# Optimization experiments

Hardware: AMD Instinct MI355X
Metric: run time of the kernel (lower is better)

## Reference

```python
import jax, jax.numpy as jnp
import numpy as np

LAYER_NUMS = 3


def setup_inputs() -> dict:
    key = jax.random.key(0)
    k1, k2 = jax.random.split(key)
    B, D = 8192, 1024
    x = jax.random.normal(k1, (B, D), dtype=jnp.float32)
    W = jax.random.normal(k2, (LAYER_NUMS, D), dtype=jnp.float32)
    b = jnp.zeros((LAYER_NUMS, D), dtype=jnp.float32)
    return {"x": x, "W": W, "b": b}


def reference(x, W, b):
    # DCN cross layer: x_{l+1} = x_0 * (x_l . w_l) + b_l + x_l
    # The torch code materializes the [B,d,d] outer product x_0 x_l^T then
    # contracts with w; algebraically identical to scaling x_0 by the
    # scalar dot product (x_l . w), which we compute directly.
    x0 = x
    x_l = x
    for i in range(LAYER_NUMS):
        scale = jnp.einsum('bd,d->b', x_l, W[i])       # [B]
        x_l = x0 * scale[:, None] + b[i][None, :] + x_l  # [B, d]
    return x_l
```

## Files before the change

### kernel.cpp

```cpp
#include <hip/hip_runtime.h>


#define DDIM 1024
#define LAYERS 3

__global__ __launch_bounds__(256) void CrossLayer_kernel(
    const float* __restrict__ x,
    const float* __restrict__ W,
    const float* __restrict__ bias,
    float* __restrict__ out,
    int B)
{
    const int wave = threadIdx.x >> 6;
    const int lane = threadIdx.x & 63;
    const int row  = blockIdx.x * 4 + wave;
    if (row >= B) return;

    const float4* xrow = reinterpret_cast<const float4*>(x + (size_t)row * DDIM);

    float4 x0[4], xl[4];
#pragma unroll
    for (int c = 0; c < 4; ++c) {
        x0[c] = xrow[c * 64 + lane];
        xl[c] = x0[c];
    }

#pragma unroll
    for (int l = 0; l < LAYERS; ++l) {
        const float4* wrow = reinterpret_cast<const float4*>(W    + l * DDIM);
        const float4* brow = reinterpret_cast<const float4*>(bias + l * DDIM);

        float partial = 0.f;
#pragma unroll
        for (int c = 0; c < 4; ++c) {
            float4 w = wrow[c * 64 + lane];
            partial += xl[c].x * w.x + xl[c].y * w.y
                     + xl[c].z * w.z + xl[c].w * w.w;
        }
#pragma unroll
        for (int off = 32; off > 0; off >>= 1)
            partial += __shfl_xor(partial, off, 64);
        const float scale = partial;

#pragma unroll
        for (int c = 0; c < 4; ++c) {
            float4 bv = brow[c * 64 + lane];
            xl[c].x = fmaf(x0[c].x, scale, bv.x + xl[c].x);
            xl[c].y = fmaf(x0[c].y, scale, bv.y + xl[c].y);
            xl[c].z = fmaf(x0[c].z, scale, bv.z + xl[c].z);
            xl[c].w = fmaf(x0[c].w, scale, bv.w + xl[c].w);
        }
    }

    float4* orow = reinterpret_cast<float4*>(out + (size_t)row * DDIM);
#pragma unroll
    for (int c = 0; c < 4; ++c)
        orow[c * 64 + lane] = xl[c];
}

extern "C" void kernel_launch(void* const* d_in, const int* in_sizes, int n_in,
                              void* d_out, int out_size, void* d_ws, size_t ws_size,
                              hipStream_t stream) {
    const float* x  = (const float*)d_in[0];
    const float* W  = (const float*)d_in[1];
    const float* b  = (const float*)d_in[2];
    float* out      = (float*)d_out;

    const int B = in_sizes[0] / DDIM;
    dim3 grid((B + 3) / 4), block(256);
    hipLaunchKernelGGL(CrossLayer_kernel, grid, block, 0, stream,
                       x, W, b, out, B);
}
```

Before: 17.53 us.

## Collapse three cross layers into one fused reduction and closed-form scale

Rewrites the layer recurrence algebraically: x_l stays of the form alpha*x0 + partial bias sums, so all three dot products (x0·w_i and the bias·w terms) are computed in one pass and reduced together. The three serialized wave reductions become one interleaved set of shuffles, and the final output is a single FMA with a summed bias. Output stores are marked nontemporal. Floating-point rounding changes slightly from the reordered arithmetic, and the bias vectors are now loaded twice.

```diff
diff --git a/kernel.cpp b/kernel.cpp
--- a/kernel.cpp
+++ b/kernel.cpp
@@ -3,6 +3,8 @@
 
 #define DDIM 1024
 #define LAYERS 3
+
+typedef float f32x4 __attribute__((ext_vector_type(4)));
 
 __global__ __launch_bounds__(256) void CrossLayer_kernel(
     const float* __restrict__ x,
@@ -16,46 +18,64 @@
     const int row  = blockIdx.x * 4 + wave;
     if (row >= B) return;
 
-    const float4* xrow = reinterpret_cast<const float4*>(x + (size_t)row * DDIM);
+    const f32x4* xrow = reinterpret_cast<const f32x4*>(x + (size_t)row * DDIM);
+    const f32x4* w0   = reinterpret_cast<const f32x4*>(W);
+    const f32x4* w1   = reinterpret_cast<const f32x4*>(W + DDIM);
+    const f32x4* w2   = reinterpret_cast<const f32x4*>(W + 2 * DDIM);
+    const f32x4* b0   = reinterpret_cast<const f32x4*>(bias);
+    const f32x4* b1   = reinterpret_cast<const f32x4*>(bias + DDIM);
+    const f32x4* b2   = reinterpret_cast<const f32x4*>(bias + 2 * DDIM);
 
-    float4 x0[4], xl[4];
+    f32x4 x0[4];
+    float d0 = 0.f, d1 = 0.f, d2 = 0.f;
+    float c1 = 0.f, c2 = 0.f;
+
 #pragma unroll
     for (int c = 0; c < 4; ++c) {
-        x0[c] = xrow[c * 64 + lane];
-        xl[c] = x0[c];
+        const int idx = c * 64 + lane;
+        f32x4 xv = xrow[idx];
+        x0[c] = xv;
+        f32x4 wv0 = w0[idx], wv1 = w1[idx], wv2 = w2[idx];
+        f32x4 bv0 = b0[idx], bv1 = b1[idx];
+
+        d0 += xv.x * wv0.x + xv.y * wv0.y + xv.z * wv0.z + xv.w * wv0.w;
+        d1 += xv.x * wv1.x + xv.y * wv1.y + xv.z * wv1.z + xv.w * wv1.w;
+        d2 += xv.x * wv2.x + xv.y * wv2.y + xv.z * wv2.z + xv.w * wv2.w;
+
+        c1 += bv0.x * wv1.x + bv0.y * wv1.y + bv0.z * wv1.z + bv0.w * wv1.w;
+        f32x4 b01 = bv0 + bv1;
+        c2 += b01.x * wv2.x + b01.y * wv2.y + b01.z * wv2.z + b01.w * wv2.w;
     }
 
 #pragma unroll
-    for (int l = 0; l < LAYERS; ++l) {
-        const float4* wrow = reinterpret_cast<const float4*>(W    + l * DDIM);
-        const float4* brow = reinterpret_cast<const float4*>(bias + l * DDIM);
-
-        float partial = 0.f;
-#pragma unroll
-        for (int c = 0; c < 4; ++c) {
-            float4 w = wrow[c * 64 + lane];
-            partial += xl[c].x * w.x + xl[c].y * w.y
-                     + xl[c].z * w.z + xl[c].w * w.w;
-        }
-#pragma unroll
-        for (int off = 32; off > 0; off >>= 1)
-            partial += __shfl_xor(partial, off, 64);
-        const float scale = partial;
-
-#pragma unroll
-        for (int c = 0; c < 4; ++c) {
-            float4 bv = brow[c * 64 + lane];
-            xl[c].x = fmaf(x0[c].x, scale, bv.x + xl[c].x);
-            xl[c].y = fmaf(x0[c].y, scale, bv.y + xl[c].y);
-            xl[c].z = fmaf(x0[c].z, scale, bv.z + xl[c].z);
-            xl[c].w = fmaf(x0[c].w, scale, bv.w + xl[c].w);
-        }
+    for (int off = 32; off > 0; off >>= 1) {
+        d0 += __shfl_xor(d0, off, 64);
+        d1 += __shfl_xor(d1, off, 64);
+        d2 += __shfl_xor(d2, off, 64);
+        c1 += __shfl_xor(c1, off, 64);
+        c2 += __shfl_xor(c2, off, 64);
     }
 
-    float4* orow = reinterpret_cast<float4*>(out + (size_t)row * DDIM);
+    const float s0 = d0;
+    const float t1 = 1.f + s0;
+    const float s1 = fmaf(t1, d1, c1);
+    const float t2 = t1 + s1;
+    const float s2 = fmaf(t2, d2, c2);
+    const float alpha = t2 + s2;
+
+    f32x4* orow = reinterpret_cast<f32x4*>(out + (size_t)row * DDIM);
 #pragma unroll
-    for (int c = 0; c < 4; ++c)
-        orow[c * 64 + lane] = xl[c];
+    for (int c = 0; c < 4; ++c) {
+        const int idx = c * 64 + lane;
+        f32x4 bv0 = b0[idx], bv1 = b1[idx], bv2 = b2[idx];
+        f32x4 bsum = bv0 + bv1 + bv2;
+        f32x4 o;
+        o.x = fmaf(x0[c].x, alpha, bsum.x);
+        o.y = fmaf(x0[c].y, alpha, bsum.y);
+        o.z = fmaf(x0[c].z, alpha, bsum.z);
+        o.w = fmaf(x0[c].w, alpha, bsum.w);
+        __builtin_nontemporal_store(o, &orow[idx]);
+    }
 }
 
 extern "C" void kernel_launch(void* const* d_in, const int* in_sizes, int n_in,
```

Measured after the change: 17.08 us. 1.03x faster.

## Collapse three cross layers into one closed-form scale and process four rows per wave

Applied to the files above, without the earlier changes.

Uses the fact that every x_l stays an affine function of x0 plus the summed biases. All three dot products against x0 are computed in one pass, bias-weight constants are precomputed, and each row's output becomes x0*alpha + sum(b). Each wave now handles four rows so the W and b loads are shared across them, and outputs use nontemporal stores. This removes the sequential per-layer reductions, at the cost of more registers per thread and fewer blocks in the grid.

```diff
diff --git a/kernel.cpp b/kernel.cpp
--- a/kernel.cpp
+++ b/kernel.cpp
@@ -2,7 +2,13 @@
 
 
 #define DDIM 1024
-#define LAYERS 3
+#define RPW 4
+
+typedef float f32x4 __attribute__((ext_vector_type(4)));
+
+__device__ __forceinline__ float dot4(f32x4 a, f32x4 b) {
+    return fmaf(a.x, b.x, fmaf(a.y, b.y, fmaf(a.z, b.z, a.w * b.w)));
+}
 
 __global__ __launch_bounds__(256) void CrossLayer_kernel(
     const float* __restrict__ x,
@@ -13,49 +19,84 @@
 {
     const int wave = threadIdx.x >> 6;
     const int lane = threadIdx.x & 63;
-    const int row  = blockIdx.x * 4 + wave;
-    if (row >= B) return;
+    const int wid  = blockIdx.x * 4 + wave;
+    const int row0 = wid * RPW;
+    if (row0 >= B) return;
 
-    const float4* xrow = reinterpret_cast<const float4*>(x + (size_t)row * DDIM);
+    const f32x4* w0 = reinterpret_cast<const f32x4*>(W);
+    const f32x4* w1 = reinterpret_cast<const f32x4*>(W + DDIM);
+    const f32x4* w2 = reinterpret_cast<const f32x4*>(W + 2 * DDIM);
+    const f32x4* b0 = reinterpret_cast<const f32x4*>(bias);
+    const f32x4* b1 = reinterpret_cast<const f32x4*>(bias + DDIM);
+    const f32x4* b2 = reinterpret_cast<const f32x4*>(bias + 2 * DDIM);
 
-    float4 x0[4], xl[4];
+    f32x4 x0[RPW][4];
+#pragma unroll
+    for (int r = 0; r < RPW; ++r) {
+        const f32x4* xr = reinterpret_cast<const f32x4*>(x + (size_t)(row0 + r) * DDIM);
+#pragma unroll
+        for (int c = 0; c < 4; ++c)
+            x0[r][c] = xr[c * 64 + lane];
+    }
+
+    f32x4 bsum[4];
+    float d[RPW][3];
+#pragma unroll
+    for (int r = 0; r < RPW; ++r) { d[r][0] = d[r][1] = d[r][2] = 0.f; }
+    float c1 = 0.f, c2 = 0.f;
+
 #pragma unroll
     for (int c = 0; c < 4; ++c) {
-        x0[c] = xrow[c * 64 + lane];
-        xl[c] = x0[c];
+        const int idx = c * 64 + lane;
+        f32x4 wv0 = w0[idx], wv1 = w1[idx], wv2 = w2[idx];
+        f32x4 bv0 = b0[idx], bv1 = b1[idx], bv2 = b2[idx];
+        bsum[c] = bv0 + bv1 + bv2;
+        c1 += dot4(bv0, wv1);
+        f32x4 b01 = bv0 + bv1;
+        c2 += dot4(b01, wv2);
+#pragma unroll
+        for (int r = 0; r < RPW; ++r) {
+            d[r][0] += dot4(x0[r][c], wv0);
+            d[r][1] += dot4(x0[r][c], wv1);
+            d[r][2] += dot4(x0[r][c], wv2);
+        }
     }
 
 #pragma unroll
-    for (int l = 0; l < LAYERS; ++l) {
-        const float4* wrow = reinterpret_cast<const float4*>(W    + l * DDIM);
-        const float4* brow = reinterpret_cast<const float4*>(bias + l * DDIM);
-
-        float partial = 0.f;
+    for (int off = 32; off > 0; off >>= 1) {
+        c1 += __shfl_xor(c1, off, 64);
+        c2 += __shfl_xor(c2, off, 64);
 #pragma unroll
-        for (int c = 0; c < 4; ++c) {
-            float4 w = wrow[c * 64 + lane];
-            partial += xl[c].x * w.x + xl[c].y * w.y
-                     + xl[c].z * w.z + xl[c].w * w.w;
-        }
-#pragma unroll
-        for (int off = 32; off > 0; off >>= 1)
-            partial += __shfl_xor(partial, off, 64);
-        const float scale = partial;
-
-#pragma unroll
-        for (int c = 0; c < 4; ++c) {
-            float4 bv = brow[c * 64 + lane];
-            xl[c].x = fmaf(x0[c].x, scale, bv.x + xl[c].x);
-            xl[c].y = fmaf(x0[c].y, scale, bv.y + xl[c].y);
-            xl[c].z = fmaf(x0[c].z, scale, bv.z + xl[c].z);
-            xl[c].w = fmaf(x0[c].w, scale, bv.w + xl[c].w);
+        for (int r = 0; r < RPW; ++r) {
+            d[r][0] += __shfl_xor(d[r][0], off, 64);
+            d[r][1] += __shfl_xor(d[r][1], off, 64);
+            d[r][2] += __shfl_xor(d[r][2], off, 64);
         }
     }
 
-    float4* orow = reinterpret_cast<float4*>(out + (size_t)row * DDIM);
+    float alpha[RPW];
 #pragma unroll
-    for (int c = 0; c < 4; ++c)
-        orow[c * 64 + lane] = xl[c];
+    for (int r = 0; r < RPW; ++r) {
+        const float t1 = 1.f + d[r][0];
+        const float s1 = fmaf(t1, d[r][1], c1);
+        const float t2 = t1 + s1;
+        const float s2 = fmaf(t2, d[r][2], c2);
+        alpha[r] = t2 + s2;
+    }
+
+#pragma unroll
+    for (int r = 0; r < RPW; ++r) {
+        f32x4* orow = reinterpret_cast<f32x4*>(out + (size_t)(row0 + r) * DDIM);
+#pragma unroll
+        for (int c = 0; c < 4; ++c) {
+            f32x4 o;
+            o.x = fmaf(x0[r][c].x, alpha[r], bsum[c].x);
+            o.y = fmaf(x0[r][c].y, alpha[r], bsum[c].y);
+            o.z = fmaf(x0[r][c].z, alpha[r], bsum[c].z);
+            o.w = fmaf(x0[r][c].w, alpha[r], bsum[c].w);
+            __builtin_nontemporal_store(o, &orow[c * 64 + lane]);
+        }
+    }
 }
 
 extern "C" void kernel_launch(void* const* d_in, const int* in_sizes, int n_in,
@@ -67,7 +108,8 @@
     float* out      = (float*)d_out;
 
     const int B = in_sizes[0] / DDIM;
-    dim3 grid((B + 3) / 4), block(256);
+    const int rows_per_block = 4 * RPW;
+    dim3 grid((B + rows_per_block - 1) / rows_per_block), block(256);
     hipLaunchKernelGGL(CrossLayer_kernel, grid, block, 0, stream,
                        x, W, b, out, B);
 }
```

Result: faster. 14.54 us (median of 2 runs) (-17.0%).
